# Optimization experiments

Hardware: AMD Instinct MI355X
Metric: run time of the kernel (lower is better)

The kernel has to match this reference:

```python
import jax, jax.numpy as jnp
import numpy as np

TOL = 1e-3

def centered_grid(h, w):
    x = jnp.arange(w, dtype=jnp.float32) - (w - 1) / 2.0
    y = jnp.arange(h, dtype=jnp.float32) - (h - 1) / 2.0
    X = jnp.broadcast_to(x[None, :], (h, w))
    Y = jnp.broadcast_to(y[:, None], (h, w))
    return X, Y

def param_to_H(p):
    B = p.shape[0]
    z = jnp.zeros((B, 1, 1), dtype=p.dtype)
    return jnp.concatenate([p, z], axis=1).reshape(B, 3, 3) + jnp.eye(3, dtype=p.dtype)

def grid_sample_bilinear(A, xn, yn):
    # torch grid_sample, mode='bilinear', align_corners=False, padding_mode='zeros'
    B, k, h, w = A.shape
    ix = ((xn + 1.0) * w - 1.0) / 2.0
    iy = ((yn + 1.0) * h - 1.0) / 2.0
    x0 = jnp.floor(ix).astype(jnp.int32); x1 = x0 + 1
    y0 = jnp.floor(iy).astype(jnp.int32); y1 = y0 + 1
    wx1 = ix - x0.astype(ix.dtype); wx0 = 1.0 - wx1
    wy1 = iy - y0.astype(iy.dtype); wy0 = 1.0 - wy1
    def gather(xi, yi):
        valid = ((xi >= 0) & (xi <= w - 1) & (yi >= 0) & (yi <= h - 1)).astype(A.dtype)
        xc = jnp.clip(xi, 0, w - 1); yc = jnp.clip(yi, 0, h - 1)
        vals = jax.vmap(lambda a, yy, xx: a[:, yy, xx])(A, yc, xc)  # [B,k,h,w]
        return vals * valid[:, None, :, :]
    out = (gather(x0, y0) * (wx0 * wy0)[:, None]
           + gather(x1, y0) * (wx1 * wy0)[:, None]
           + gather(x0, y1) * (wx0 * wy1)[:, None]
           + gather(x1, y1) * (wx1 * wy1)[:, None])
    return out

def warp_hmg(img, p):
    B, k, h, w = img.shape
    X, Y = centered_grid(h, w)
    xy = jnp.stack([X.reshape(-1), Y.reshape(-1), jnp.ones(h * w, jnp.float32)], 0)  # [3,hw]
    H = param_to_H(p)
    xyw = jnp.einsum('bij,jn->bin', H, xy)
    Xw = (xyw[:, 0] / xyw[:, 2]).reshape(B, h, w) + (w - 1) / 2.0
    Yw = (xyw[:, 1] / xyw[:, 2]).reshape(B, h, w) + (h - 1) / 2.0
    xn = Xw / ((w - 1) / 2.0) - 1.0
    yn = Yw / ((h - 1) / 2.0) - 1.0
    Q = grid_sample_bilinear(img, xn, yn)
    mask = ((xn > -1 + 2.0 / w) & (xn < 1 - 2.0 / w)
            & (yn > -1 + 2.0 / h) & (yn < 1 - 2.0 / h)).astype(img.dtype)
    return Q, mask

def image_gradients(img):
    # central differences with replicate padding (matches GradientBatch)
    px = jnp.pad(img, ((0, 0), (0, 0), (0, 0), (1, 1)), mode='edge')
    dx = 0.5 * (px[..., 2:] - px[..., :-2])
    py = jnp.pad(img, ((0, 0), (0, 0), (1, 1), (0, 0)), mode='edge')
    dy = 0.5 * (py[..., 2:, :] - py[..., :-2, :])
    return dx, dy

def compute_dIdp(gx, gy):
    B, k, h, w = gx.shape
    X, Y = centered_grid(h, w)
    Xf = jnp.tile(X.reshape(-1), k)  # [k*h*w]
    Yf = jnp.tile(Y.reshape(-1), k)
    gx = gx.reshape(B, k * h * w)
    gy = gy.reshape(B, k * h * w)
    cols = [Xf * gx, Yf * gx, gx, Xf * gy, Yf * gy, gy,
            -Xf * Xf * gx - Xf * Yf * gy, -Xf * Yf * gx - Yf * Yf * gy]
    return jnp.stack(cols, axis=2)  # [B, k*h*w, 8]

def deeplk_forward(img, temp, max_itr):
    Fi, Ft = img, temp
    B, k, h, w = Ft.shape
    gx, gy = image_gradients(Ft)
    dIdp = compute_dIdp(gx, gy)                      # [B, N, 8]
    invH = jnp.linalg.inv(jnp.einsum('bni,bnj->bij', dIdp, dIdp))  # [B,8,8]
    invH_dIdp = jnp.einsum('bij,bnj->bin', invH, dIdp)             # [B,8,N]
    p0 = jnp.zeros((B, 8, 1), jnp.float32)
    dp0 = jnp.ones((B, 8, 1), jnp.float32)

    def step(carry, _):
        p, dp = carry
        Fi_warp, mask = warp_hmg(Fi, p)
        r = (Fi_warp - Ft * mask[:, None]).reshape(B, -1, 1)
        dp_new = jnp.einsum('bin,bnj->bij', invH_dIdp, r)
        dp_new = dp_new.at[:, 6:8, 0].set(0.0)
        cond = (jnp.linalg.norm(dp, axis=1, keepdims=True) > TOL).astype(p.dtype)
        dp2 = cond * dp_new  # per-sample gate: once converged dp stays 0 (matches torch while-loop)
        return (p - dp2, dp2), None

    (p, _), _ = jax.lax.scan(step, (p0, dp0), None, length=int(max_itr))
    return p, param_to_H(p)

def setup_inputs() -> dict:
    key = jax.random.key(0)
    k1, k2 = jax.random.split(key)
    img = jax.random.normal(k1, (16, 3, 256, 256), jnp.float32)
    temp = jax.random.normal(k2, (16, 3, 256, 256), jnp.float32)
    return {"img": img, "temp": temp, "max_itr": 20}

def reference(img, temp, max_itr):
    return deeplk_forward(img, temp, max_itr)
```

## Files before the change

### kernel.cpp

```cpp
#include <hip/hip_runtime.h>

#define BATCH 16
#define KCH 3
#define IH 256
#define IW 256
#define NPIX (IH*IW)
#define NITER 20
#define HCH 64
#define CH 16
#define SSLOTS 64
#define TPBF 256
#define TPBM 1024
#define NBLK (BATCH*CH)

#define AGENT __HIP_MEMORY_SCOPE_AGENT

struct Ws {
    float  hess_part[BATCH][HCH][36];
    double invH[BATCH][64];
    double s_part[2][BATCH][SSLOTS][8];
    double p[2][BATCH][8];
    double dpn2[2][BATCH];
    int    cnt[NITER][BATCH][32];
};

__device__ __forceinline__ double aload_d(const double* p) {
    return __hip_atomic_load(p, __ATOMIC_RELAXED, AGENT);
}
__device__ __forceinline__ void astore_d(double* p, double v) {
    __hip_atomic_store(p, v, __ATOMIC_RELAXED, AGENT);
}

__device__ __forceinline__ void pixel_accum(const float* __restrict__ I,
                                            const float* __restrict__ T,
                                            int x, int y,
                                            float h00, float h01, float h02,
                                            float h10, float h11, float h12,
                                            float* acc8, float* acc36, bool do_hess) {
    const float XL = -1.f + 2.f / IW, XH = 1.f - 2.f / IW;
    const float YL = -1.f + 2.f / IH, YH = 1.f - 2.f / IH;
    float X = (float)x - 127.5f, Y = (float)y - 127.5f;

    float Xw = (h00 * X + h01 * Y + h02) + 127.5f;
    float Yw = (h10 * X + h11 * Y + h12) + 127.5f;
    float xn = Xw / 127.5f - 1.f;
    float yn = Yw / 127.5f - 1.f;

    float ix = ((xn + 1.f) * (float)IW - 1.f) * 0.5f;
    float iy = ((yn + 1.f) * (float)IH - 1.f) * 0.5f;
    float fx0 = floorf(ix), fy0 = floorf(iy);
    int x0 = (int)fx0, y0 = (int)fy0;
    int x1 = x0 + 1, y1 = y0 + 1;
    float wx1 = ix - fx0, wx0 = 1.f - wx1;
    float wy1 = iy - fy0, wy0 = 1.f - wy1;

    bool vx0 = (x0 >= 0) && (x0 <= IW - 1), vx1 = (x1 >= 0) && (x1 <= IW - 1);
    bool vy0 = (y0 >= 0) && (y0 <= IH - 1), vy1 = (y1 >= 0) && (y1 <= IH - 1);
    int xc0 = min(max(x0, 0), IW - 1), xc1 = min(max(x1, 0), IW - 1);
    int yc0 = min(max(y0, 0), IH - 1), yc1 = min(max(y1, 0), IH - 1);

    float w00 = (wx0 * wy0) * ((vx0 && vy0) ? 1.f : 0.f);
    float w10 = (wx1 * wy0) * ((vx1 && vy0) ? 1.f : 0.f);
    float w01 = (wx0 * wy1) * ((vx0 && vy1) ? 1.f : 0.f);
    float w11 = (wx1 * wy1) * ((vx1 && vy1) ? 1.f : 0.f);

    float mask = (xn > XL && xn < XH && yn > YL && yn < YH) ? 1.f : 0.f;

#pragma unroll
    for (int c = 0; c < KCH; c++) {
        const float* Ic = I + c * NPIX;
        const float* Tc = T + c * NPIX;
        float v00 = Ic[yc0 * IW + xc0];
        float v10 = Ic[yc0 * IW + xc1];
        float v01 = Ic[yc1 * IW + xc0];
        float v11 = Ic[yc1 * IW + xc1];
        float Q = v00 * w00 + v10 * w10 + v01 * w01 + v11 * w11;
        float r = Q - Tc[y * IW + x] * mask;
        float gx = 0.5f * (Tc[y * IW + min(x + 1, IW - 1)] - Tc[y * IW + max(x - 1, 0)]);
        float gy = 0.5f * (Tc[min(y + 1, IH - 1) * IW + x] - Tc[max(y - 1, 0) * IW + x]);
        float gxr = gx * r, gyr = gy * r;
        float ur = X * gxr + Y * gyr;
        acc8[0] += X * gxr;
        acc8[1] += Y * gxr;
        acc8[2] += gxr;
        acc8[3] += X * gyr;
        acc8[4] += Y * gyr;
        acc8[5] += gyr;
        acc8[6] -= X * ur;
        acc8[7] -= Y * ur;
        if (do_hess) {
            float d[8];
            d[0] = X * gx; d[1] = Y * gx; d[2] = gx;
            d[3] = X * gy; d[4] = Y * gy; d[5] = gy;
            d[6] = -X * X * gx - X * Y * gy;
            d[7] = -X * Y * gx - Y * Y * gy;
            int idx = 0;
#pragma unroll
            for (int i = 0; i < 8; i++)
#pragma unroll
                for (int j = i; j < 8; j++) { acc36[idx] += d[i] * d[j]; idx++; }
        }
    }
}

__global__ __launch_bounds__(TPBF) void k_first(const float* __restrict__ img,
                                                const float* __restrict__ temp, Ws* ws) {
    const int b = blockIdx.y, chunk = blockIdx.x, t = threadIdx.x;
    const int lane = t & 63, wave = t >> 6;
    float acc8[8], acc36[36];
#pragma unroll
    for (int i = 0; i < 8; i++) acc8[i] = 0.f;
#pragma unroll
    for (int i = 0; i < 36; i++) acc36[i] = 0.f;
    const float* I = img + (size_t)b * KCH * NPIX;
    const float* T = temp + (size_t)b * KCH * NPIX;

#pragma unroll
    for (int pp = 0; pp < 4; ++pp)
        pixel_accum(I, T, t, chunk * 4 + pp, 1.f, 0.f, 0.f, 0.f, 1.f, 0.f,
                    acc8, acc36, true);

#pragma unroll
    for (int i = 0; i < 36; i++) {
        float v = acc36[i];
        for (int o = 32; o > 0; o >>= 1) v += __shfl_xor(v, o, 64);
        acc36[i] = v;
    }
#pragma unroll
    for (int i = 0; i < 8; i++) {
        float v = acc8[i];
        for (int o = 32; o > 0; o >>= 1) v += __shfl_xor(v, o, 64);
        acc8[i] = v;
    }
    __shared__ float red36[4][36];
    __shared__ float red8[4][8];
    if (lane == 0) {
#pragma unroll
        for (int i = 0; i < 36; i++) red36[wave][i] = acc36[i];
#pragma unroll
        for (int i = 0; i < 8; i++) red8[wave][i] = acc8[i];
    }
    __syncthreads();
    if (t < 36)
        ws->hess_part[b][chunk][t] = red36[0][t] + red36[1][t] + red36[2][t] + red36[3][t];
    if (t < 8)
        ws->s_part[0][b][chunk][t] =
            (double)(red8[0][t] + red8[1][t] + red8[2][t] + red8[3][t]);
}

__global__ __launch_bounds__(1024) void k_invert(Ws* ws) {
    const int t = threadIdx.x;
    {
        int* c = &ws->cnt[0][0][0];
        const int total = NITER * BATCH * 32;
        for (int i = t; i < total; i += 1024) c[i] = 0;
    }
    const int b = t >> 6, lane = t & 63;
    double hv = 0.0;
    if (lane < 36) {
        for (int c = 0; c < HCH; c++) hv += (double)ws->hess_part[b][c][lane];
    }
    const int ii = lane >> 3, jj = lane & 7;
    const int a = min(ii, jj), bb = max(ii, jj);
    const int pidx = a * 8 - a * (a - 1) / 2 + (bb - a);
    double Mv = __shfl(hv, pidx, 64);
    double Av = (ii == jj) ? 1.0 : 0.0;
#pragma unroll
    for (int k = 0; k < 8; k++) {
        double pivd = __shfl(Mv, k * 8 + k, 64);
        double inv = 1.0 / pivd;
        double rM = __shfl(Mv, k * 8 + jj, 64) * inv;
        double rA = __shfl(Av, k * 8 + jj, 64) * inv;
        double fac = __shfl(Mv, ii * 8 + k, 64);
        if (ii == k) { Mv = rM; Av = rA; }
        else         { Mv -= fac * rM; Av -= fac * rA; }
    }
    ws->invH[b][lane] = Av;
}

__device__ __forceinline__ void batchbar(Ws* ws, int it, int b) {
    asm volatile("s_waitcnt vmcnt(0)" ::: "memory");
    __syncthreads();
    if (threadIdx.x == 0) {
        __hip_atomic_fetch_add(&ws->cnt[it][b][0], 1, __ATOMIC_RELAXED, AGENT);
        while (__hip_atomic_load(&ws->cnt[it][b][0], __ATOMIC_RELAXED, AGENT) < CH)
            __builtin_amdgcn_s_sleep(4);
    }
    __syncthreads();
    asm volatile("" ::: "memory");
}

__global__ __launch_bounds__(TPBM) void mega_loop(const float* __restrict__ img,
                                                  const float* __restrict__ temp,
                                                  Ws* ws, float* __restrict__ out) {
    const int bid = blockIdx.x;
    const int b = bid & 15;
    const int chunk = bid >> 4;
    const int t = threadIdx.x;
    const int lane = t & 63, wave = t >> 6;
    const int x = t & 255, yrow = t >> 8;

    __shared__ double ir_sh[64];
    __shared__ float red8[16][8];

    const float* I = img + (size_t)b * KCH * NPIX;
    const float* T = temp + (size_t)b * KCH * NPIX;

    if (t < 64) ir_sh[t] = ws->invH[b][t];
    __syncthreads();

    float tcv[4][KCH], gxv[4][KCH], gyv[4][KCH];
#pragma unroll
    for (int pp = 0; pp < 4; ++pp) {
        const int y = chunk * 16 + yrow * 4 + pp;
        const int ym = max(y - 1, 0), yp = min(y + 1, IH - 1);
        const int xm = max(x - 1, 0), xp = min(x + 1, IW - 1);
#pragma unroll
        for (int c = 0; c < KCH; c++) {
            const float* Tc = T + c * NPIX;
            tcv[pp][c] = Tc[y * IW + x];
            gxv[pp][c] = 0.5f * (Tc[y * IW + xp] - Tc[y * IW + xm]);
            gyv[pp][c] = 0.5f * (Tc[yp * IW + x] - Tc[ym * IW + x]);
        }
    }

    const float XL = -1.f + 2.f / IW, XH = 1.f - 2.f / IW;
    const float YL = -1.f + 2.f / IH, YH = 1.f - 2.f / IH;
    const float Xc = (float)x - 127.5f;

    double p_reg = 0.0, dpn2 = 8.0;
    for (int it = 1; it <= NITER; ++it) {
        {
            const int par = (it - 1) & 1;
            const int j = lane & 7, c_lo = lane >> 3;
            const int nm = (it == 1) ? 8 : 2;
            double sv = 0.0;
            for (int m = 0; m < nm; m++)
                sv += aload_d(&ws->s_part[par][b][c_lo + 8 * m][j]);
            sv += __shfl_xor(sv, 8, 64);
            sv += __shfl_xor(sv, 16, 64);
            sv += __shfl_xor(sv, 32, 64);
            double dp = 0.0;
#pragma unroll
            for (int jj = 0; jj < 8; jj++)
                dp += ir_sh[(lane & 7) * 8 + jj] * __shfl(sv, jj, 64);
            double d = (lane < 6 && dpn2 > 1e-6) ? dp : 0.0;
            double n2 = d * d;
            n2 += __shfl_xor(n2, 1, 64);
            n2 += __shfl_xor(n2, 2, 64);
            n2 += __shfl_xor(n2, 4, 64);
            p_reg -= d;
            dpn2 = n2;
        }
        if (it == NITER) break;

        float pf[8];
#pragma unroll
        for (int jj = 0; jj < 8; jj++) pf[jj] = (float)__shfl(p_reg, jj, 64);
        const float h00 = 1.f + pf[0], h01 = pf[1], h02 = pf[2];
        const float h10 = pf[3], h11 = 1.f + pf[4], h12 = pf[5];

        float acc8[8];
#pragma unroll
        for (int i = 0; i < 8; i++) acc8[i] = 0.f;

#pragma unroll
        for (int pp = 0; pp < 4; ++pp) {
            const int y = chunk * 16 + yrow * 4 + pp;
            const float Y = (float)y - 127.5f;

            float Xw = (h00 * Xc + h01 * Y + h02) + 127.5f;
            float Yw = (h10 * Xc + h11 * Y + h12) + 127.5f;
            float xn = Xw / 127.5f - 1.f;
            float yn = Yw / 127.5f - 1.f;

            float ix = ((xn + 1.f) * (float)IW - 1.f) * 0.5f;
            float iy = ((yn + 1.f) * (float)IH - 1.f) * 0.5f;
            float fx0 = floorf(ix), fy0 = floorf(iy);
            int x0 = (int)fx0, y0 = (int)fy0;
            int x1 = x0 + 1, y1 = y0 + 1;
            float wx1 = ix - fx0, wx0 = 1.f - wx1;
            float wy1 = iy - fy0, wy0 = 1.f - wy1;

            bool vx0 = (x0 >= 0) && (x0 <= IW - 1), vx1 = (x1 >= 0) && (x1 <= IW - 1);
            bool vy0 = (y0 >= 0) && (y0 <= IH - 1), vy1 = (y1 >= 0) && (y1 <= IH - 1);
            int xc0 = min(max(x0, 0), IW - 1), xc1 = min(max(x1, 0), IW - 1);
            int yc0 = min(max(y0, 0), IH - 1), yc1 = min(max(y1, 0), IH - 1);

            float w00 = (wx0 * wy0) * ((vx0 && vy0) ? 1.f : 0.f);
            float w10 = (wx1 * wy0) * ((vx1 && vy0) ? 1.f : 0.f);
            float w01 = (wx0 * wy1) * ((vx0 && vy1) ? 1.f : 0.f);
            float w11 = (wx1 * wy1) * ((vx1 && vy1) ? 1.f : 0.f);

            float mask = (xn > XL && xn < XH && yn > YL && yn < YH) ? 1.f : 0.f;

#pragma unroll
            for (int c = 0; c < KCH; c++) {
                const float* Ic = I + c * NPIX;
                float v00 = Ic[yc0 * IW + xc0];
                float v10 = Ic[yc0 * IW + xc1];
                float v01 = Ic[yc1 * IW + xc0];
                float v11 = Ic[yc1 * IW + xc1];
                float Q = v00 * w00 + v10 * w10 + v01 * w01 + v11 * w11;
                float r = Q - tcv[pp][c] * mask;
                float gxr = gxv[pp][c] * r, gyr = gyv[pp][c] * r;
                float ur = Xc * gxr + Y * gyr;
                acc8[0] += Xc * gxr;
                acc8[1] += Y * gxr;
                acc8[2] += gxr;
                acc8[3] += Xc * gyr;
                acc8[4] += Y * gyr;
                acc8[5] += gyr;
                acc8[6] -= Xc * ur;
                acc8[7] -= Y * ur;
            }
        }

#pragma unroll
        for (int i = 0; i < 8; i++) {
            float v = acc8[i];
            for (int o = 32; o > 0; o >>= 1) v += __shfl_xor(v, o, 64);
            acc8[i] = v;
        }
        if (lane == 0) {
#pragma unroll
            for (int i = 0; i < 8; i++) red8[wave][i] = acc8[i];
        }
        __syncthreads();
        if (t < 8) {
            float tot = 0.f;
#pragma unroll
            for (int w = 0; w < 16; w++) tot += red8[w][t];
            astore_d(&ws->s_part[it & 1][b][chunk][t], (double)tot);
        }
        batchbar(ws, it, b);
    }

    if (chunk == 0 && wave == 0) {
        if (lane < 8) {
            out[b * 8 + lane] = (float)p_reg;
            out[128 + b * 9 + lane] =
                (float)(p_reg + ((lane == 0 || lane == 4) ? 1.0 : 0.0));
        }
        if (lane == 8) out[128 + b * 9 + 8] = 1.0f;
    }
}

__device__ __forceinline__ double do_update_ws(const Ws* ws, int b, int it, int lane,
                                               double* n2_out) {
    const int par = (it - 1) & 1;
    const int j = lane & 7, c_lo = lane >> 3;
    double sv = 0.0;
#pragma unroll
    for (int m = 0; m < 8; m++) sv += ws->s_part[par][b][c_lo + 8 * m][j];
    sv += __shfl_xor(sv, 8, 64);
    sv += __shfl_xor(sv, 16, 64);
    sv += __shfl_xor(sv, 32, 64);
    const double* row = &ws->invH[b][(lane & 7) * 8];
    double dp = 0.0;
#pragma unroll
    for (int jj = 0; jj < 8; jj++) dp += row[jj] * __shfl(sv, jj, 64);
    double p_prev = 0.0, dpn2_prev = 8.0;
    if (it > 1) {
        if (lane < 8) p_prev = ws->p[par][b][lane];
        dpn2_prev = ws->dpn2[par][b];
    }
    double d = (lane < 6 && dpn2_prev > 1e-6) ? dp : 0.0;
    double n2 = d * d;
    n2 += __shfl_xor(n2, 1, 64);
    n2 += __shfl_xor(n2, 2, 64);
    n2 += __shfl_xor(n2, 4, 64);
    *n2_out = n2;
    return p_prev - d;
}

__global__ __launch_bounds__(TPBF) void k_iter(const float* __restrict__ img,
                                               const float* __restrict__ temp,
                                               Ws* ws, int it) {
    const int b = blockIdx.y, chunk = blockIdx.x, t = threadIdx.x;
    const int lane = t & 63, wave = t >> 6;
    double n2;
    double p_cur = do_update_ws(ws, b, it, lane, &n2);
    float pf[8];
#pragma unroll
    for (int jj = 0; jj < 8; jj++) pf[jj] = (float)__shfl(p_cur, jj, 64);
    if (chunk == 0 && wave == 0) {
        if (lane < 8) ws->p[it & 1][b][lane] = p_cur;
        if (lane == 0) ws->dpn2[it & 1][b] = n2;
    }
    float acc8[8];
#pragma unroll
    for (int i = 0; i < 8; i++) acc8[i] = 0.f;
    const float* I = img + (size_t)b * KCH * NPIX;
    const float* T = temp + (size_t)b * KCH * NPIX;
#pragma unroll
    for (int pp = 0; pp < 4; ++pp)
        pixel_accum(I, T, t, chunk * 4 + pp,
                    1.f + pf[0], pf[1], pf[2], pf[3], 1.f + pf[4], pf[5],
                    acc8, nullptr, false);
#pragma unroll
    for (int i = 0; i < 8; i++) {
        float v = acc8[i];
        for (int o = 32; o > 0; o >>= 1) v += __shfl_xor(v, o, 64);
        acc8[i] = v;
    }
    __shared__ float red8[4][8];
    if (lane == 0) {
#pragma unroll
        for (int i = 0; i < 8; i++) red8[wave][i] = acc8[i];
    }
    __syncthreads();
    if (t < 8)
        ws->s_part[it & 1][b][chunk][t] =
            (double)(red8[0][t] + red8[1][t] + red8[2][t] + red8[3][t]);
}

__global__ __launch_bounds__(1024) void k_out(Ws* ws, float* __restrict__ out) {
    const int t = threadIdx.x;
    const int b = t >> 6, lane = t & 63;
    double n2;
    double p_fin = do_update_ws(ws, b, NITER, lane, &n2);
    if (lane < 8) {
        out[b * 8 + lane] = (float)p_fin;
        out[128 + b * 9 + lane] =
            (float)(p_fin + ((lane == 0 || lane == 4) ? 1.0 : 0.0));
    }
    if (lane == 8) out[128 + b * 9 + 8] = 1.0f;
}

extern "C" void kernel_launch(void* const* d_in, const int* in_sizes, int n_in,
                              void* d_out, int out_size, void* d_ws, size_t ws_size,
                              hipStream_t stream) {
    const float* img  = (const float*)d_in[0];
    const float* temp = (const float*)d_in[1];
    Ws* ws = (Ws*)d_ws;
    float* out = (float*)d_out;

    k_first<<<dim3(HCH, BATCH), TPBF, 0, stream>>>(img, temp, ws);
    k_invert<<<1, 1024, 0, stream>>>(ws);

    int dev = 0, nCU = 0, maxB = 0;
    hipGetDevice(&dev);
    hipDeviceGetAttribute(&nCU, hipDeviceAttributeMultiprocessorCount, dev);
    hipError_t e = hipOccupancyMaxActiveBlocksPerMultiprocessor(
        &maxB, (const void*)mega_loop, TPBM, 0);
    const bool coop_ok = (e == hipSuccess) && ((long)maxB * nCU >= NBLK);

    if (coop_ok) {
        void* args[] = {(void*)&img, (void*)&temp, (void*)&ws, (void*)&out};
        hipLaunchCooperativeKernel((void*)mega_loop, dim3(NBLK), dim3(TPBM), args, 0,
                                   stream);
    } else {
        for (int it = 1; it < NITER; ++it)
            k_iter<<<dim3(HCH, BATCH), TPBF, 0, stream>>>(img, temp, ws, it);
        k_out<<<1, 1024, 0, stream>>>(ws, out);
    }
}
```

Baseline: 216.1 us.

## Replace per-iteration batch barrier with per-chunk flags and algebraic accumulator reduction

The per-iteration atomic-counter barrier is replaced by per-chunk progress flags. Each block polls all 16 chunk flags of its batch with a wave vote and reads partial sums from a triple-buffered slot, so there is no counter reset or fetch-add per iteration. The 8 gradient accumulators are factored into 5 per-pixel sums, with X-dependent terms applied once after the loop. The warp coordinates are computed incrementally in pixel units, and the inverse Hessian row is kept in registers instead of shared memory. This cuts synchronization latency and ALU work, but changes the mask comparison form and float rounding slightly.

```diff
diff --git a/kernel.cpp b/kernel.cpp
--- a/kernel.cpp
+++ b/kernel.cpp
@@ -8,7 +8,6 @@
 #define NITER 20
 #define HCH 64
 #define CH 16
-#define SSLOTS 64
 #define TPBF 256
 #define TPBM 1024
 #define NBLK (BATCH*CH)
@@ -18,10 +17,12 @@
 struct Ws {
     float  hess_part[BATCH][HCH][36];
     double invH[BATCH][64];
-    double s_part[2][BATCH][SSLOTS][8];
+    double s0[BATCH][HCH][8];
+    double s_part[3][BATCH][CH][8];
+    double sfb[2][BATCH][HCH][8];
     double p[2][BATCH][8];
     double dpn2[2][BATCH];
-    int    cnt[NITER][BATCH][32];
+    int    flags[BATCH][CH];
 };
 
 __device__ __forceinline__ double aload_d(const double* p) {
@@ -144,17 +145,13 @@
     if (t < 36)
         ws->hess_part[b][chunk][t] = red36[0][t] + red36[1][t] + red36[2][t] + red36[3][t];
     if (t < 8)
-        ws->s_part[0][b][chunk][t] =
+        ws->s0[b][chunk][t] =
             (double)(red8[0][t] + red8[1][t] + red8[2][t] + red8[3][t]);
 }
 
 __global__ __launch_bounds__(1024) void k_invert(Ws* ws) {
     const int t = threadIdx.x;
-    {
-        int* c = &ws->cnt[0][0][0];
-        const int total = NITER * BATCH * 32;
-        for (int i = t; i < total; i += 1024) c[i] = 0;
-    }
+    if (t < BATCH * CH) (&ws->flags[0][0])[t] = 0;
     const int b = t >> 6, lane = t & 63;
     double hv = 0.0;
     if (lane < 36) {
@@ -176,18 +173,6 @@
         else         { Mv -= fac * rM; Av -= fac * rA; }
     }
     ws->invH[b][lane] = Av;
-}
-
-__device__ __forceinline__ void batchbar(Ws* ws, int it, int b) {
-    asm volatile("s_waitcnt vmcnt(0)" ::: "memory");
-    __syncthreads();
-    if (threadIdx.x == 0) {
-        __hip_atomic_fetch_add(&ws->cnt[it][b][0], 1, __ATOMIC_RELAXED, AGENT);
-        while (__hip_atomic_load(&ws->cnt[it][b][0], __ATOMIC_RELAXED, AGENT) < CH)
-            __builtin_amdgcn_s_sleep(4);
-    }
-    __syncthreads();
-    asm volatile("" ::: "memory");
 }
 
 __global__ __launch_bounds__(TPBM) void mega_loop(const float* __restrict__ img,
@@ -200,14 +185,14 @@
     const int lane = t & 63, wave = t >> 6;
     const int x = t & 255, yrow = t >> 8;
 
-    __shared__ double ir_sh[64];
     __shared__ float red8[16][8];
 
     const float* I = img + (size_t)b * KCH * NPIX;
     const float* T = temp + (size_t)b * KCH * NPIX;
 
-    if (t < 64) ir_sh[t] = ws->invH[b][t];
-    __syncthreads();
+    double ir[8];
+#pragma unroll
+    for (int j = 0; j < 8; j++) ir[j] = ws->invH[b][(lane & 7) * 8 + j];
 
     float tcv[4][KCH], gxv[4][KCH], gyv[4][KCH];
 #pragma unroll
@@ -224,26 +209,38 @@
         }
     }
 
-    const float XL = -1.f + 2.f / IW, XH = 1.f - 2.f / IW;
-    const float YL = -1.f + 2.f / IH, YH = 1.f - 2.f / IH;
+    const float S = 256.0f / 255.0f;
     const float Xc = (float)x - 127.5f;
+    const float Y0 = (float)(chunk * 16 + yrow * 4) - 127.5f;
 
     double p_reg = 0.0, dpn2 = 8.0;
     for (int it = 1; it <= NITER; ++it) {
         {
-            const int par = (it - 1) & 1;
             const int j = lane & 7, c_lo = lane >> 3;
-            const int nm = (it == 1) ? 8 : 2;
             double sv = 0.0;
-            for (int m = 0; m < nm; m++)
-                sv += aload_d(&ws->s_part[par][b][c_lo + 8 * m][j]);
+            if (it == 1) {
+#pragma unroll
+                for (int m = 0; m < 8; m++)
+                    sv += aload_d(&ws->s0[b][c_lo + 8 * m][j]);
+            } else {
+                const int need = it - 1;
+                const int fidx = lane & 15;
+                while (true) {
+                    int fl = __hip_atomic_load(&ws->flags[b][fidx],
+                                               __ATOMIC_RELAXED, AGENT);
+                    if (__all(fl >= need)) break;
+                    __builtin_amdgcn_s_sleep(1);
+                }
+                const double* sp = &ws->s_part[(it - 1) % 3][b][0][0];
+                sv = aload_d(sp + c_lo * 8 + j) + aload_d(sp + (c_lo + 8) * 8 + j);
+            }
             sv += __shfl_xor(sv, 8, 64);
             sv += __shfl_xor(sv, 16, 64);
             sv += __shfl_xor(sv, 32, 64);
             double dp = 0.0;
 #pragma unroll
             for (int jj = 0; jj < 8; jj++)
-                dp += ir_sh[(lane & 7) * 8 + jj] * __shfl(sv, jj, 64);
+                dp += ir[jj] * __shfl(sv, jj, 64);
             double d = (lane < 6 && dpn2 > 1e-6) ? dp : 0.0;
             double n2 = d * d;
             n2 += __shfl_xor(n2, 1, 64);
@@ -260,22 +257,18 @@
         const float h00 = 1.f + pf[0], h01 = pf[1], h02 = pf[2];
         const float h10 = pf[3], h11 = 1.f + pf[4], h12 = pf[5];
 
-        float acc8[8];
-#pragma unroll
-        for (int i = 0; i < 8; i++) acc8[i] = 0.f;
+        const float ix0 = (h00 * Xc + h01 * Y0 + h02 + 127.5f) * S - 0.5f;
+        const float iy0 = (h10 * Xc + h11 * Y0 + h12 + 127.5f) * S - 0.5f;
+        const float dix = h01 * S, diy = h11 * S;
+
+        float G1 = 0.f, G1Y = 0.f, G2 = 0.f, G2Y = 0.f, G2YY = 0.f;
 
 #pragma unroll
         for (int pp = 0; pp < 4; ++pp) {
-            const int y = chunk * 16 + yrow * 4 + pp;
-            const float Y = (float)y - 127.5f;
-
-            float Xw = (h00 * Xc + h01 * Y + h02) + 127.5f;
-            float Yw = (h10 * Xc + h11 * Y + h12) + 127.5f;
-            float xn = Xw / 127.5f - 1.f;
-            float yn = Yw / 127.5f - 1.f;
-
-            float ix = ((xn + 1.f) * (float)IW - 1.f) * 0.5f;
-            float iy = ((yn + 1.f) * (float)IH - 1.f) * 0.5f;
+            const float Y = Y0 + (float)pp;
+            const float ix = ix0 + (float)pp * dix;
+            const float iy = iy0 + (float)pp * diy;
+
             float fx0 = floorf(ix), fy0 = floorf(iy);
             int x0 = (int)fx0, y0 = (int)fy0;
             int x1 = x0 + 1, y1 = y0 + 1;
@@ -292,7 +285,9 @@
             float w01 = (wx0 * wy1) * ((vx0 && vy1) ? 1.f : 0.f);
             float w11 = (wx1 * wy1) * ((vx1 && vy1) ? 1.f : 0.f);
 
-            float mask = (xn > XL && xn < XH && yn > YL && yn < YH) ? 1.f : 0.f;
+            float mask = (ix > 0.5f && ix < 254.5f && iy > 0.5f && iy < 254.5f)
+                         ? 1.f : 0.f;
+            const float Y2 = Y * Y;
 
 #pragma unroll
             for (int c = 0; c < KCH; c++) {
@@ -304,17 +299,23 @@
                 float Q = v00 * w00 + v10 * w10 + v01 * w01 + v11 * w11;
                 float r = Q - tcv[pp][c] * mask;
                 float gxr = gxv[pp][c] * r, gyr = gyv[pp][c] * r;
-                float ur = Xc * gxr + Y * gyr;
-                acc8[0] += Xc * gxr;
-                acc8[1] += Y * gxr;
-                acc8[2] += gxr;
-                acc8[3] += Xc * gyr;
-                acc8[4] += Y * gyr;
-                acc8[5] += gyr;
-                acc8[6] -= Xc * ur;
-                acc8[7] -= Y * ur;
+                G1  += gxr;
+                G1Y += Y * gxr;
+                G2  += gyr;
+                G2Y += Y * gyr;
+                G2YY += Y2 * gyr;
             }
         }
+
+        float acc8[8];
+        acc8[0] = Xc * G1;
+        acc8[1] = G1Y;
+        acc8[2] = G1;
+        acc8[3] = Xc * G2;
+        acc8[4] = G2Y;
+        acc8[5] = G2;
+        acc8[6] = -Xc * (Xc * G1 + G2Y);
+        acc8[7] = -(Xc * G1Y + G2YY);
 
 #pragma unroll
         for (int i = 0; i < 8; i++) {
@@ -331,9 +332,12 @@
             float tot = 0.f;
 #pragma unroll
             for (int w = 0; w < 16; w++) tot += red8[w][t];
-            astore_d(&ws->s_part[it & 1][b][chunk][t], (double)tot);
-        }
-        batchbar(ws, it, b);
+            astore_d(&ws->s_part[it % 3][b][chunk][t], (double)tot);
+        }
+        asm volatile("s_waitcnt vmcnt(0)" ::: "memory");
+        __syncthreads();
+        if (t == 0)
+            __hip_atomic_store(&ws->flags[b][chunk], it, __ATOMIC_RELAXED, AGENT);
     }
 
     if (chunk == 0 && wave == 0) {
@@ -348,11 +352,12 @@
 
 __device__ __forceinline__ double do_update_ws(const Ws* ws, int b, int it, int lane,
                                                double* n2_out) {
-    const int par = (it - 1) & 1;
     const int j = lane & 7, c_lo = lane >> 3;
+    const double* base = (it == 1) ? &ws->s0[b][0][0]
+                                   : &ws->sfb[(it - 1) & 1][b][0][0];
     double sv = 0.0;
 #pragma unroll
-    for (int m = 0; m < 8; m++) sv += ws->s_part[par][b][c_lo + 8 * m][j];
+    for (int m = 0; m < 8; m++) sv += base[(c_lo + 8 * m) * 8 + j];
     sv += __shfl_xor(sv, 8, 64);
     sv += __shfl_xor(sv, 16, 64);
     sv += __shfl_xor(sv, 32, 64);
@@ -362,8 +367,8 @@
     for (int jj = 0; jj < 8; jj++) dp += row[jj] * __shfl(sv, jj, 64);
     double p_prev = 0.0, dpn2_prev = 8.0;
     if (it > 1) {
-        if (lane < 8) p_prev = ws->p[par][b][lane];
-        dpn2_prev = ws->dpn2[par][b];
+        if (lane < 8) p_prev = ws->p[(it - 1) & 1][b][lane];
+        dpn2_prev = ws->dpn2[(it - 1) & 1][b];
     }
     double d = (lane < 6 && dpn2_prev > 1e-6) ? dp : 0.0;
     double n2 = d * d;
@@ -411,7 +416,7 @@
     }
     __syncthreads();
     if (t < 8)
-        ws->s_part[it & 1][b][chunk][t] =
+        ws->sfb[it & 1][b][chunk][t] =
             (double)(red8[0][t] + red8[1][t] + red8[2][t] + red8[3][t]);
 }
 
```

New measurement: 220.9 us. +2.2%, slower.
